# Optimization experiments

Measured on AMD Instinct MI355X. Metric: run time of the kernel, lower is better.

Reference implementation:

```python
import jax, jax.numpy as jnp
import numpy as np
from jax import lax

D_MODEL = 200
N_LAYER = 12
NHEADS = 8
HEADDIM = 50
D_STATE = 64
D_INNER = 2 * D_MODEL            # 400
CONV_DIM = D_INNER + 2 * D_STATE  # 528 (ngroups=1)
D_IN_PROJ = 2 * D_INNER + 2 * D_STATE + NHEADS  # 936
D_CONV = 4
EPS = 1e-5


def rmsnorm(x, w):
    v = jnp.mean(jnp.square(x), axis=-1, keepdims=True)
    return x * lax.rsqrt(v + EPS) * w


def groupnorm(x, groups, g, b):
    B, C, H, W = x.shape
    xg = x.reshape(B, groups, C // groups, H, W)
    mu = jnp.mean(xg, axis=(2, 3, 4), keepdims=True)
    var = jnp.mean(jnp.square(xg - mu), axis=(2, 3, 4), keepdims=True)
    xn = ((xg - mu) * lax.rsqrt(var + EPS)).reshape(B, C, H, W)
    return xn * g[:, None, None] + b[:, None, None]


def patch_embed(x, pe_conv_w, proj_in_w, gn_g, gn_b, spec_w):
    b, c, l, d = x.shape
    # time path: 'b c l d' -> (b, 1, c*l, d), conv -> (b, 25, c*l, 8)
    time_x = x.reshape(b, 1, c * l, d)
    t = lax.conv_general_dilated(time_x, proj_in_w, (1, 25), ((0, 0), (24, 24)),
                                 dimension_numbers=('NCHW', 'OIHW', 'NCHW'))
    t = jax.nn.gelu(groupnorm(t, 5, gn_g, gn_b), approximate=False)
    time_emb = t.transpose(0, 2, 1, 3).reshape(b, c, l, D_MODEL)
    # freq path: rfft over patch dim, norm='forward'
    spec = jnp.abs(jnp.fft.rfft(x, axis=-1, norm='forward'))  # (b,c,l,101)
    spec_emb = jnp.einsum('bclf,df->bcld', spec, spec_w)
    patch = time_emb + spec_emb
    # depthwise 7x7 positional conv over (d, c, l)
    pos = lax.conv_general_dilated(patch.transpose(0, 3, 1, 2), pe_conv_w, (1, 1),
                                   ((3, 3), (3, 3)),
                                   dimension_numbers=('NCHW', 'OIHW', 'NCHW'),
                                   feature_group_count=D_MODEL)
    return patch + pos.transpose(0, 2, 3, 1)


def ssd_scan(xh, dt, B, C, A, D):
    # xh: (b,l,h,p)  dt: (b,l,h)  B,C: (b,l,n)  A,D: (h,)
    b, l, h, p = xh.shape

    def step(state, inp):
        x_t, dt_t, B_t, C_t = inp
        dA = jnp.exp(dt_t * A)  # (b,h)
        state = state * dA[:, :, None, None] + \
            (dt_t[:, :, None, None] * x_t[:, :, :, None]) * B_t[:, None, None, :]
        y = jnp.einsum('bhpn,bn->bhp', state, C_t)
        return state, y

    state0 = jnp.zeros((b, h, p, D_STATE), xh.dtype)
    _, ys = lax.scan(step, state0,
                     (xh.transpose(1, 0, 2, 3), dt.transpose(1, 0, 2),
                      B.transpose(1, 0, 2), C.transpose(1, 0, 2)))
    return ys.transpose(1, 0, 2, 3) + xh * D[None, None, :, None]


def mamba2(u, in_w, conv_w, conv_b, dt_bias, A_log, D, gn_w, out_w):
    b, l, _ = u.shape
    zxbcdt = u @ in_w.T  # (b,l,936)
    z = zxbcdt[..., :D_INNER]
    xBC = zxbcdt[..., D_INNER:D_INNER + CONV_DIM]
    dt = jax.nn.softplus(zxbcdt[..., D_INNER + CONV_DIM:] + dt_bias)  # (b,l,8)
    # causal depthwise conv1d, kernel 4
    xc = lax.conv_general_dilated(xBC.transpose(0, 2, 1), conv_w, (1,), ((D_CONV - 1, 0),),
                                  dimension_numbers=('NCH', 'OIH', 'NCH'),
                                  feature_group_count=CONV_DIM)
    xBC = jax.nn.silu((xc + conv_b[:, None]).transpose(0, 2, 1))
    x = xBC[..., :D_INNER].reshape(b, l, NHEADS, HEADDIM)
    Bm = xBC[..., D_INNER:D_INNER + D_STATE]
    Cm = xBC[..., D_INNER + D_STATE:]
    y = ssd_scan(x, dt, Bm, Cm, -jnp.exp(A_log), D).reshape(b, l, D_INNER)
    y = rmsnorm(y * jax.nn.silu(z), gn_w)  # RMSNormGated, norm_before_gate=False
    return y @ out_w.T


@jax.checkpoint
def layer(hidden, residual, norm_w, in_w, conv_w, conv_b, dt_bias, A_log, D, gn_w, out_w):
    residual = hidden + residual
    hidden = mamba2(rmsnorm(residual, norm_w), in_w, conv_w, conv_b, dt_bias, A_log, D, gn_w, out_w)
    return hidden, residual


def forward(x, pe_conv_w, proj_in_w, gn_g, gn_b, spec_w, norm_w, in_proj_w, conv_w, conv_b,
            dt_bias, A_log, D, gnorm_w, out_proj_w, norm_f_w, head_w, head_b):
    b, c, l, d = x.shape
    hidden = patch_embed(x, pe_conv_w, proj_in_w, gn_g, gn_b, spec_w).reshape(b, c * l, d)
    residual = jnp.zeros_like(hidden)
    for i in range(N_LAYER):
        hidden, residual = layer(hidden, residual, norm_w[i], in_proj_w[i], conv_w[i],
                                 conv_b[i], dt_bias[i], A_log[i], D[i], gnorm_w[i], out_proj_w[i])
    hidden = rmsnorm(hidden + residual, norm_f_w).reshape(b, c, l, d)
    return hidden @ head_w.T + head_b


def setup_inputs():
    key = jax.random.key(0)
    ks = jax.random.split(key, 12)
    B, CH, L, P = 16, 19, 30, 200

    def g(k, shape, scale):
        return jax.random.normal(k, shape, jnp.float32) * scale

    dt = jax.random.uniform(ks[8], (N_LAYER, NHEADS), jnp.float32, 1e-3, 0.1)
    return {
        'x': g(ks[0], (B, CH, L, P), 1.0),
        'pe_conv_w': g(ks[1], (D_MODEL, 1, 7, 7), 0.15),
        'proj_in_w': g(ks[2], (25, 1, 1, 49), 0.14),
        'gn_g': jnp.ones(25, jnp.float32),
        'gn_b': jnp.zeros(25, jnp.float32),
        'spec_w': g(ks[3], (D_MODEL, 101), 0.1),
        'norm_w': jnp.ones((N_LAYER, D_MODEL), jnp.float32),
        'in_proj_w': g(ks[4], (N_LAYER, D_IN_PROJ, D_MODEL), 0.07),
        'conv_w': g(ks[5], (N_LAYER, CONV_DIM, 1, D_CONV), 0.4),
        'conv_b': jnp.zeros((N_LAYER, CONV_DIM), jnp.float32),
        'dt_bias': jnp.log(jnp.expm1(dt)),
        'A_log': jnp.log(jax.random.uniform(ks[9], (N_LAYER, NHEADS), jnp.float32, 1.0, 16.0)),
        'D': jnp.ones((N_LAYER, NHEADS), jnp.float32),
        'gnorm_w': jnp.ones((N_LAYER, D_INNER), jnp.float32),
        'out_proj_w': g(ks[6], (N_LAYER, D_MODEL, D_INNER), 0.05),
        'norm_f_w': jnp.ones(D_MODEL, jnp.float32),
        'head_w': g(ks[7], (D_MODEL, D_MODEL), 0.07),
        'head_b': jnp.zeros(D_MODEL, jnp.float32),
    }


def reference(x, pe_conv_w, proj_in_w, gn_g, gn_b, spec_w, norm_w, in_proj_w, conv_w, conv_b,
              dt_bias, A_log, D, gnorm_w, out_proj_w, norm_f_w, head_w, head_b):
    return forward(x, pe_conv_w, proj_in_w, gn_g, gn_b, spec_w, norm_w, in_proj_w, conv_w,
                   conv_b, dt_bias, A_log, D, gnorm_w, out_proj_w, norm_f_w, head_w, head_b)
```

## Files before the change

kernel.cpp:

```cpp
#include <hip/hip_runtime.h>
#include <hip/hip_bf16.h>
#include <math.h>

#define D_MODEL   200
#define N_LAYER   12
#define NHEADS    8
#define HEADDIM   50
#define D_STATE   64
#define D_INNER   400
#define CONV_DIM  528
#define D_IN_PROJ 936
#define D_CONV    4
#define EPS       1e-5f

#define BATCH 16
#define CH    19
#define LLEN  30
#define SEQ   570
#define NTOK  9120
#define NFREQ 101

typedef __attribute__((ext_vector_type(8))) short s8v;
typedef __attribute__((ext_vector_type(4))) float f32x4;

// ... 168 lines not shown
}

__global__ __launch_bounds__(256) void time_conv_kernel(
    const float* __restrict__ x, const float* __restrict__ pw,
    float* __restrict__ traw)
{
    int br = blockIdx.x;
    __shared__ float xr[200];
    if (threadIdx.x < 200) xr[threadIdx.x] = x[(size_t)br * 200 + threadIdx.x];
    __syncthreads();
    if (threadIdx.x < 200) {
        int oc = threadIdx.x >> 3, j = threadIdx.x & 7;
        int start = j * 25 - 24;
        float acc = 0.f;
#pragma unroll
        for (int k = 0; k < 49; k++) {
            int d = start + k;
            if (d >= 0 && d < 200) acc = fmaf(xr[d], pw[oc * 49 + k], acc);
        }
        int b = br / SEQ, row = br % SEQ;
        traw[(((size_t)b * 25 + oc) * SEQ + row) * 8 + j] = acc;
    }
}

__global__ __launch_bounds__(256) void gn_stats_kernel(
    const float* __restrict__ traw, float* __restrict__ stats)
{
    int bg = blockIdx.x;
    int b = bg / 5, g = bg % 5;
    const float* base = traw + ((size_t)b * 25 + g * 5) * SEQ * 8;
    float s = 0.f, q = 0.f;
    for (int i = threadIdx.x; i < 5 * SEQ * 8; i += 256) {
        float v = base[i];
        s += v; q = fmaf(v, v, q);
    }
    __shared__ float rs[4], rq[4];
    int lane = threadIdx.x & 63, w = threadIdx.x >> 6;
#pragma unroll
    for (int o = 32; o; o >>= 1) { s += __shfl_xor(s, o, 64); q += __shfl_xor(q, o, 64); }
    if (lane == 0) { rs[w] = s; rq[w] = q; }
    __syncthreads();
    if (threadIdx.x == 0) {
        float S = rs[0] + rs[1] + rs[2] + rs[3];
        float Q = rq[0] + rq[1] + rq[2] + rq[3];
        float inv = 1.f / (5.f * SEQ * 8.f);
        float mean = S * inv;
        float var = Q * inv - mean * mean;
        stats[bg * 2] = mean;
        stats[bg * 2 + 1] = rsqrtf(var + EPS);
    }
}

__global__ __launch_bounds__(256) void gn_gelu_kernel(
    const float* __restrict__ traw, const float* __restrict__ stats,
    const float* __restrict__ gn_g, const float* __restrict__ gn_b,
    float* __restrict__ patch)
{
    int idx = blockIdx.x * 256 + threadIdx.x;
    if (idx >= NTOK * 200) return;
    int d = idx % 200;
    int row = (idx / 200) % SEQ;
    int b = idx / (200 * SEQ);
    int oc = d >> 3, j = d & 7;
    float v = traw[(((size_t)b * 25 + oc) * SEQ + row) * 8 + j];
    int g = oc / 5;
    float mean = stats[(b * 5 + g) * 2];
    float rstd = stats[(b * 5 + g) * 2 + 1];
    v = (v - mean) * rstd * gn_g[oc] + gn_b[oc];
    float ge = 0.5f * v * (1.f + erff(v * 0.70710678118654752f));
    patch[idx] = ge;
}

__global__ __launch_bounds__(256) void dft_init_kernel(float* __restrict__ CS)
{
    int idx = blockIdx.x * 256 + threadIdx.x;
    if (idx >= 202 * 200) return;
    int f = idx / 200, d = idx % 200;
    int fr = (f < NFREQ) ? f : (f - NFREQ);
    int m = (fr * d) % 200;
    float ang = -6.283185307179586f * (float)m * (1.f / 200.f);
    CS[idx] = (f < NFREQ) ? cosf(ang) : sinf(ang);
}

__global__ __launch_bounds__(256) void dft_init_bf_kernel(short* __restrict__ CS)
{
    int idx = blockIdx.x * 256 + threadIdx.x;
    if (idx >= 202 * 224) return;
    int f = idx / 224, d = idx - f * 224;
    short out = 0;
    if (d < 200) {
        int fr = (f < NFREQ) ? f : (f - NFREQ);
        int m = (fr * d) % 200;
        float ang = -6.283185307179586f * (float)m * (1.f / 200.f);
        out = f2bf((f < NFREQ) ? cosf(ang) : sinf(ang));
    }
    CS[idx] = out;
}

__global__ __launch_bounds__(256) void mag_kernel(
    const float* __restrict__ cs_out, float* __restrict__ magv)
{
    int idx = blockIdx.x * 256 + threadIdx.x;
    if (idx >= NTOK * NFREQ) return;
    int m = idx / NFREQ, f = idx % NFREQ;
    float re = cs_out[(size_t)m * 202 + f];
    float im = cs_out[(size_t)m * 202 + NFREQ + f];
    magv[idx] = sqrtf(re * re + im * im) * 0.005f;
}

__global__ __launch_bounds__(256) void mag_bf_kernel(
    const float* __restrict__ cs_out, short* __restrict__ magv)
{
    int idx = blockIdx.x * 256 + threadIdx.x;
    if (idx >= NTOK * 128) return;
    int m = idx >> 7, f = idx & 127;
    short out = 0;
    if (f < NFREQ) {
        float re = cs_out[(size_t)m * 202 + f];
        float im = cs_out[(size_t)m * 202 + NFREQ + f];
        out = f2bf(sqrtf(re * re + im * im) * 0.005f);
    }
    magv[idx] = out;
}

__global__ __launch_bounds__(256) void pe_conv3_kernel(
    const float* __restrict__ patch, const float* __restrict__ pw,
    float* __restrict__ hidden)
{
    int b = blockIdx.x, dc = blockIdx.y, ct = blockIdx.z;
    int d0 = dc * 16, c0 = ct * 4;
    __shared__ float pl[10 * 30 * 16];
    __shared__ float wl[49 * 16];
    int tid = threadIdx.x;
    int dd = tid & 15;
    int d = d0 + dd;

    for (int i = tid; i < 10 * 30 * 16; i += 256) {
        int ddl = i & 15, r = i >> 4;
        int l = r % 30, cr = r / 30;
        int cc = c0 + cr - 3, dl = d0 + ddl;
        pl[i] = (cc >= 0 && cc < CH && dl < 200)
                    ? patch[((size_t)(b * CH + cc) * LLEN + l) * 200 + dl] : 0.f;
    }
    for (int i = tid; i < 49 * 16; i += 256) {
        int k = i >> 4, dl = d0 + (i & 15);
        wl[i] = (dl < 200) ? pw[(size_t)dl * 49 + k] : 0.f;
    }
    __syncthreads();

    float wreg[49];
#pragma unroll
    for (int k = 0; k < 49; k++) wreg[k] = wl[k * 16 + dd];

    for (int o = tid; o < 4 * 30 * 16; o += 256) {
        int r2 = o >> 4;
        int l = r2 % 30, ci = r2 / 30;
        int c = c0 + ci;
        if (c >= CH) continue;
        float acc = pl[((ci + 3) * 30 + l) * 16 + dd];
#pragma unroll
        for (int i = 0; i < 7; i++) {
#pragma unroll
            for (int j = 0; j < 7; j++) {
                int ll = l + j - 3;
                if (ll < 0 || ll >= LLEN) continue;
                acc = fmaf(pl[((ci + i) * 30 + ll) * 16 + dd], wreg[i * 7 + j], acc);
            }
        }
        if (d < 200) hidden[((size_t)(b * CH + c) * LLEN + l) * 200 + d] = acc;
    }
}

__global__ __launch_bounds__(64) void add_rmsnorm_kernel(
    const float* __restrict__ hidden, float* __restrict__ residual,
    const float* __restrict__ wn, float* __restrict__ u,
    short* __restrict__ ubf, int first)
{
    int m = blockIdx.x;
    int lane = threadIdx.x;
    const float* hr = hidden + (size_t)m * 200;
    float* rr = residual + (size_t)m * 200;
    float v[4];
    float ss = 0.f;
#pragma unroll
    for (int i = 0; i < 4; i++) {
        int k = lane + i * 64;
        float xv = 0.f;
        if (k < 200) {
            xv = hr[k] + (first ? 0.f : rr[k]);
            rr[k] = xv;
        }
        v[i] = xv;
        ss = fmaf(xv, xv, ss);
    }
#pragma unroll
    for (int o = 32; o; o >>= 1) ss += __shfl_xor(ss, o, 64);
    float rstd = rsqrtf(ss * (1.f / 200.f) + EPS);
#pragma unroll
    for (int i = 0; i < 4; i++) {
        int k = lane + i * 64;
        float val = v[i] * rstd * ((k < 200) ? wn[k] : 0.f);
        if (k < 200 && u) u[(size_t)m * 200 + k] = val;
        if (ubf) {
            if (k < 200) ubf[(size_t)m * 224 + k] = f2bf(val);
            else if (k < 224) ubf[(size_t)m * 224 + k] = 0;
        }
    }
}

__global__ __launch_bounds__(256) void norm_dt_kernel(
    const float* __restrict__ hidden, float* __restrict__ residual,
    const float* __restrict__ wn, short* __restrict__ ubf,
    const float* __restrict__ Win, const float* __restrict__ dt_bias,
    float* __restrict__ dtb, int layer, int first)
{
    int m = blockIdx.x;
    int tid = threadIdx.x;
    __shared__ float su[200];
    __shared__ float rs[4];
    float xv = 0.f;
    if (tid < 200) {
        xv = hidden[(size_t)m * 200 + tid] + (first ? 0.f : residual[(size_t)m * 200 + tid]);
        residual[(size_t)m * 200 + tid] = xv;
    }
    float ss = xv * xv;
#pragma unroll
    for (int o = 32; o; o >>= 1) ss += __shfl_xor(ss, o, 64);
    int lane = tid & 63, w = tid >> 6;
    if (lane == 0) rs[w] = ss;
    __syncthreads();
    float rstd = rsqrtf((rs[0] + rs[1] + rs[2] + rs[3]) * (1.f / 200.f) + EPS);
    if (tid < 200) {
        float val = xv * rstd * wn[tid];
        su[tid] = val;
        ubf[(size_t)m * 224 + tid] = f2bf(val);
    } else if (tid < 224) {
        ubf[(size_t)m * 224 + tid] = 0;
    }
    __syncthreads();
    int h = tid >> 5, l = tid & 31;
    const float* wr = Win + (size_t)layer * D_IN_PROJ * 200 + (size_t)(928 + h) * 200;
    float s = 0.f;
    for (int k = l; k < 200; k += 32) s = fmaf(su[k], wr[k], s);
    s += __shfl_xor(s, 16, 32);
    s += __shfl_xor(s, 8, 32);
    s += __shfl_xor(s, 4, 32);
    s += __shfl_xor(s, 2, 32);
    s += __shfl_xor(s, 1, 32);
    if (l == 0) {
        float raw = s + dt_bias[layer * NHEADS + h];
        dtb[(size_t)m * NHEADS + h] = (raw > 20.f) ? raw : log1pf(expf(raw));
    }
}

__global__ __launch_bounds__(256) void dt_gemv_kernel(
    const float* __restrict__ u, const float* __restrict__ Win,
    const float* __restrict__ dt_bias, float* __restrict__ dtb, int layer)
{
    int tid = threadIdx.x;
    int tok = blockIdx.x * 4 + (tid >> 6);
    int head = (tid >> 3) & 7;
    int l8 = tid & 7;
    const float* ur = u + (size_t)tok * 200;
    const float* wr = Win + (size_t)layer * D_IN_PROJ * 200 + (size_t)(928 + head) * 200;
    float s = 0.f;
    for (int k = l8; k < 200; k += 8) s = fmaf(ur[k], wr[k], s);
    s += __shfl_xor(s, 1, 64);
    s += __shfl_xor(s, 2, 64);
    s += __shfl_xor(s, 4, 64);
    if (l8 == 0) {
        float raw = s + dt_bias[layer * NHEADS + head];
        dtb[(size_t)tok * NHEADS + head] = (raw > 20.f) ? raw : log1pf(expf(raw));
    }
}

__global__ __launch_bounds__(256) void dtconv2_kernel(
    const float* __restrict__ zxbcdt, const float* __restrict__ cw,
    const float* __restrict__ cb, float* __restrict__ xBC, int layer)
{
    int b = blockIdx.x, tt = blockIdx.y;
    int t0 = tt * 8;
    __shared__ float zs[11][528];
    const float* cwl = cw + (size_t)layer * CONV_DIM * 4;
    const float* cbl = cb + (size_t)layer * CONV_DIM;
    for (int i = threadIdx.x; i < 11 * 528; i += 256) {
        int r = i / 528, ch = i - r * 528;
        int t = t0 - 3 + r;
        zs[r][ch] = (t >= 0 && t < SEQ)
                        ? zxbcdt[(size_t)(b * SEQ + t) * D_IN_PROJ + D_INNER + ch] : 0.f;
    }
    __syncthreads();
    for (int o = threadIdx.x; o < 8 * 528; o += 256) {
        int tr = o / 528, ch = o - tr * 528;
        int t = t0 + tr;
        if (t >= SEQ) continue;
        float acc = cbl[ch];
#pragma unroll
        for (int k = 0; k < 4; k++)
            acc = fmaf(zs[tr + k][ch], cwl[ch * 4 + k], acc);
        xBC[(size_t)(b * SEQ + t) * CONV_DIM + ch] = acc / (1.f + __expf(-acc));
    }
}

__global__ __launch_bounds__(256) void ssd_state4_kernel(
    const float* __restrict__ xBC, const float* __restrict__ dtb,
    const float* __restrict__ A_log, float* __restrict__ Sbuf,
    float* __restrict__ Pd, int layer, int lchunk, int nchunk)
{
    int b = blockIdx.x, c = blockIdx.y, bz = blockIdx.z;
    int tid = threadIdx.x;
    int hl = tid >> 6, p = tid & 63;
    int h = bz * 4 + hl;
    float A = -expf(A_log[layer * NHEADS + h]);

    __shared__ __align__(16) float sh[2][2][272];
    int t0 = c * lchunk;
    int npairs = lchunk >> 1, rem = lchunk & 1;

    {
        if (tid < 132) {
            int tok = (tid >= 66) ? 1 : 0;
            int fidx = tid - tok * 66;
            int g = (fidx < 50) ? (50 * bz + fidx) : (fidx + 50);
            float4 v = ((const float4*)(xBC + (size_t)(b * SEQ + t0 + tok) * CONV_DIM))[g];
            *(float4*)&sh[0][tok][fidx * 4] = v;
        } else if (tid < 140) {
            int e = tid - 132, tok = e >> 2, hd = e & 3;
            sh[0][tok][264 + hd] = dtb[(size_t)(b * SEQ + t0 + tok) * NHEADS + bz * 4 + hd];
        }
    }
    __syncthreads();

    float s[64];
#pragma unroll
    for (int n = 0; n < 64; n++) s[n] = 0.f;
    float pacc = 1.f;

    for (int i = 0; i < npairs; i++) {
        int t = t0 + 2 * i;
        int buf = i & 1, nb = buf ^ 1;
        bool pf = (2 * i + 2 < lchunk);
        float4 rx;
        float rdt = 0.f;
        int tok = 0, fidx = 0;
        if (pf) {
            if (tid < 132) {
                tok = (tid >= 66) ? 1 : 0;
                fidx = tid - tok * 66;
                int tq = t + 2 + tok; if (tq > SEQ - 1) tq = SEQ - 1;
                int g = (fidx < 50) ? (50 * bz + fidx) : (fidx + 50);
                rx = ((const float4*)(xBC + (size_t)(b * SEQ + tq) * CONV_DIM))[g];
            } else if (tid < 140) {
                int e = tid - 132, tk = e >> 2, hd = e & 3;
                int tq = t + 2 + tk; if (tq > SEQ - 1) tq = SEQ - 1;
                rdt = dtb[(size_t)(b * SEQ + tq) * NHEADS + bz * 4 + hd];
            }
        }
#pragma unroll
        for (int k = 0; k < 2; k++) {
            float dtv = sh[buf][k][264 + hl];
            float xp  = (p < HEADDIM) ? sh[buf][k][hl * HEADDIM + p] : 0.f;
            float dA = __expf(dtv * A);
            float u  = dtv * xp;
            pacc *= dA;
            const float4* B4 = (const float4*)&sh[buf][k][200];
#pragma unroll
            for (int n4 = 0; n4 < 16; n4++) {
                float4 bq = B4[n4];
                s[4 * n4 + 0] = fmaf(s[4 * n4 + 0], dA, u * bq.x);
                s[4 * n4 + 1] = fmaf(s[4 * n4 + 1], dA, u * bq.y);
                s[4 * n4 + 2] = fmaf(s[4 * n4 + 2], dA, u * bq.z);
                s[4 * n4 + 3] = fmaf(s[4 * n4 + 3], dA, u * bq.w);
            }
        }
        if (pf) {
            if (tid < 132) *(float4*)&sh[nb][tok][fidx * 4] = rx;
            else if (tid < 140) { int e = tid - 132; sh[nb][e >> 2][264 + (e & 3)] = rdt; }
        }
        __syncthreads();
    }

    if (rem) {
        int buf = npairs & 1;
        float dtv = sh[buf][0][264 + hl];
        float xp  = (p < HEADDIM) ? sh[buf][0][hl * HEADDIM + p] : 0.f;
        float dA = __expf(dtv * A);
        float u  = dtv * xp;
        pacc *= dA;
        const float4* B4 = (const float4*)&sh[buf][0][200];
#pragma unroll
        for (int n4 = 0; n4 < 16; n4++) {
            float4 bq = B4[n4];
            s[4 * n4 + 0] = fmaf(s[4 * n4 + 0], dA, u * bq.x);
            s[4 * n4 + 1] = fmaf(s[4 * n4 + 1], dA, u * bq.y);
            s[4 * n4 + 2] = fmaf(s[4 * n4 + 2], dA, u * bq.z);
            s[4 * n4 + 3] = fmaf(s[4 * n4 + 3], dA, u * bq.w);
        }
    }

    if (p < HEADDIM) {
        float* Sb = Sbuf + ((size_t)((b * NHEADS + h) * nchunk + c)) * (HEADDIM * 64)
                    + p * 64;
#pragma unroll
        for (int n4 = 0; n4 < 16; n4++)
            ((float4*)Sb)[n4] = make_float4(s[4 * n4], s[4 * n4 + 1],
                                            s[4 * n4 + 2], s[4 * n4 + 3]);
    }
    if (p == 0) Pd[(b * NHEADS + h) * nchunk + c] = pacc;
}

__global__ __launch_bounds__(512) void ssd_state_kernel(
    const float* __restrict__ xBC, const float* __restrict__ dtb,
    const float* __restrict__ A_log, float* __restrict__ Sbuf,
    float* __restrict__ Pd, int layer, int lchunk, int nchunk)
{
    int b = blockIdx.x, c = blockIdx.y;
    int tid = threadIdx.x;
    int h = tid >> 6, p = tid & 63;
    float A = -expf(A_log[layer * NHEADS + h]);

    __shared__ float sh[2][544];
    int t0 = c * lchunk, tend = t0 + lchunk;

    {
        const float* base = xBC + (size_t)(b * SEQ + t0) * CONV_DIM;
        sh[0][tid] = base[tid];
        if (tid < 24) {
            int e2 = 512 + tid;
            sh[0][e2] = (e2 < 528) ? base[e2]
                                   : dtb[(size_t)(b * SEQ + t0) * NHEADS + (e2 - 528)];
        }
    }
    __syncthreads();

    float s[64];
#pragma unroll
    for (int n = 0; n < 64; n++) s[n] = 0.f;
    float pacc = 1.f;

    for (int t = t0; t < tend; t++) {
        int cur = (t - t0) & 1, nxt = cur ^ 1;
        float pf0 = 0.f, pf1 = 0.f;
        if (t + 1 < tend) {
            const float* base = xBC + (size_t)(b * SEQ + t + 1) * CONV_DIM;
            pf0 = base[tid];
            if (tid < 24) {
                int e2 = 512 + tid;
                pf1 = (e2 < 528) ? base[e2]
                                 : dtb[(size_t)(b * SEQ + t + 1) * NHEADS + (e2 - 528)];
            }
        }
        float dtv = sh[cur][528 + h];
        float xp  = (p < HEADDIM) ? sh[cur][h * HEADDIM + p] : 0.f;
        float dA = __expf(dtv * A);
        float u  = dtv * xp;
        pacc *= dA;
        const float4* B4 = (const float4*)&sh[cur][D_INNER];
#pragma unroll
        for (int n4 = 0; n4 < 16; n4++) {
            float4 bq = B4[n4];
            s[4 * n4 + 0] = fmaf(s[4 * n4 + 0], dA, u * bq.x);
            s[4 * n4 + 1] = fmaf(s[4 * n4 + 1], dA, u * bq.y);
            s[4 * n4 + 2] = fmaf(s[4 * n4 + 2], dA, u * bq.z);
            s[4 * n4 + 3] = fmaf(s[4 * n4 + 3], dA, u * bq.w);
        }
        if (t + 1 < tend) {
            sh[nxt][tid] = pf0;
            if (tid < 24) sh[nxt][512 + tid] = pf1;
        }
        __syncthreads();
    }

    if (p < HEADDIM) {
        float* Sb = Sbuf + ((size_t)((b * NHEADS + h) * nchunk + c)) * (HEADDIM * 64)
                    + p * 64;
#pragma unroll
        for (int n4 = 0; n4 < 16; n4++)
            ((float4*)Sb)[n4] = make_float4(s[4 * n4], s[4 * n4 + 1],
                                            s[4 * n4 + 2], s[4 * n4 + 3]);
    }
    if (p == 0) Pd[(b * NHEADS + h) * nchunk + c] = pacc;
}

__global__ __launch_bounds__(256) void ssd_scan2b_kernel(
    float* __restrict__ Sbuf, const float* __restrict__ Pd, int nchunk)
{
    int bh = blockIdx.x;
    int e = blockIdx.y * 256 + threadIdx.x;
    if (e >= HEADDIM * 64) return;
    float* base = Sbuf + (size_t)bh * nchunk * (HEADDIM * 64) + e;
    const float* pd = Pd + bh * nchunk;
    float cur = 0.f;
    for (int c = 0; c < nchunk; c++) {
        float l = base[(size_t)c * (HEADDIM * 64)];
        base[(size_t)c * (HEADDIM * 64)] = cur;
        cur = fmaf(pd[c], cur, l);
    }
}

__global__ __launch_bounds__(256) void ssd_out5_kernel(
    const float* __restrict__ xBC, const float* __restrict__ dtb,
    const float* __restrict__ zxbcdt, const float* __restrict__ A_log,
    const float* __restrict__ Dv, const float* __restrict__ Sbuf,
    const float* __restrict__ gw, short* __restrict__ ybf,
    float* __restrict__ ssq, int layer, int lchunk, int nchunk)
{
    int b = blockIdx.x, c = blockIdx.y, bz = blockIdx.z;
    int tid = threadIdx.x;
    int hl = tid >> 6, p = tid & 63;
    int h = bz * 4 + hl;
    float A = -expf(A_log[layer * NHEADS + h]);
    float Dh = Dv[layer * NHEADS + h];
    float gval = (p < HEADDIM) ? gw[(size_t)layer * D_INNER + h * HEADDIM + p] : 0.f;

    __shared__ __align__(16) float sh[2][2][336];
    __shared__ __align__(16) float shz[2][2][200];
    __shared__ float red[2][2][4];
    int t0 = c * lchunk;
    int npairs = lchunk >> 1;

    {
        if (tid < 164) {
            int tok = (tid >= 82) ? 1 : 0;
            int fidx = tid - tok * 82;
            int g = (fidx < 50) ? (50 * bz + fidx) : (fidx + 50);
            float4 v = ((const float4*)(xBC + (size_t)(b * SEQ + t0 + tok) * CONV_DIM))[g];
            *(float4*)&sh[0][tok][fidx * 4] = v;
        } else if (tid < 172) {
            int e = tid - 164, tok = e >> 2, hd = e & 3;
            sh[0][tok][328 + hd] = dtb[(size_t)(b * SEQ + t0 + tok) * NHEADS + bz * 4 + hd];
        }
        if (tid < 100) {
            int tok = (tid >= 50) ? 1 : 0;
            int fz = tid - tok * 50;
            float4 v = ((const float4*)(zxbcdt + (size_t)(b * SEQ + t0 + tok) * D_IN_PROJ))[50 * bz + fz];
            *(float4*)&shz[0][tok][fz * 4] = v;
        }
    }

    float s[64];
    if (p < HEADDIM) {
        const float* Sb = Sbuf + ((size_t)((b * NHEADS + h) * nchunk + c)) * (HEADDIM * 64)
                          + p * 64;
#pragma unroll
        for (int n4 = 0; n4 < 16; n4++) {
            float4 v = ((const float4*)Sb)[n4];
            s[4 * n4] = v.x; s[4 * n4 + 1] = v.y; s[4 * n4 + 2] = v.z; s[4 * n4 + 3] = v.w;
        }
    } else {
#pragma unroll
        for (int n = 0; n < 64; n++) s[n] = 0.f;
    }
    __syncthreads();

    for (int i = 0; i < npairs; i++) {
        int t = t0 + 2 * i;
        int buf = i & 1, nb = buf ^ 1;
        bool pf = (2 * i + 2 < lchunk);
        float4 rx, rz;
        float rdt = 0.f;
        int xtok = 0, xf = 0, ztok = 0, zf = 0;
        if (pf) {
            if (tid < 164) {
                xtok = (tid >= 82) ? 1 : 0;
                xf = tid - xtok * 82;
                int tq = t + 2 + xtok; if (tq > SEQ - 1) tq = SEQ - 1;
                int g = (xf < 50) ? (50 * bz + xf) : (xf + 50);
                rx = ((const float4*)(xBC + (size_t)(b * SEQ + tq) * CONV_DIM))[g];
            } else if (tid < 172) {
                int e = tid - 164, tk = e >> 2, hd = e & 3;
                int tq = t + 2 + tk; if (tq > SEQ - 1) tq = SEQ - 1;
                rdt = dtb[(size_t)(b * SEQ + tq) * NHEADS + bz * 4 + hd];
            }
            if (tid < 100) {
                ztok = (tid >= 50) ? 1 : 0;
                zf = tid - ztok * 50;
                int tq = t + 2 + ztok; if (tq > SEQ - 1) tq = SEQ - 1;
                rz = ((const float4*)(zxbcdt + (size_t)(b * SEQ + tq) * D_IN_PROJ))[50 * bz + zf];
            }
        }
        float g0 = 0.f, g1 = 0.f;
#pragma unroll
        for (int k = 0; k < 2; k++) {
            float dtv = sh[buf][k][328 + hl];
            float xp  = (p < HEADDIM) ? sh[buf][k][hl * HEADDIM + p] : 0.f;
            float dA = __expf(dtv * A);
            float u  = dtv * xp;
            const float4* B4 = (const float4*)&sh[buf][k][200];
            const float4* C4 = (const float4*)&sh[buf][k][264];
            float y0 = 0.f, y1 = 0.f, y2 = 0.f, y3 = 0.f;
#pragma unroll
            for (int n4 = 0; n4 < 16; n4++) {
                float4 bq = B4[n4];
                float4 cq = C4[n4];
                float t0v = fmaf(s[4 * n4 + 0], dA, u * bq.x);
                float t1v = fmaf(s[4 * n4 + 1], dA, u * bq.y);
                float t2v = fmaf(s[4 * n4 + 2], dA, u * bq.z);
                float t3v = fmaf(s[4 * n4 + 3], dA, u * bq.w);
                s[4 * n4 + 0] = t0v; s[4 * n4 + 1] = t1v;
                s[4 * n4 + 2] = t2v; s[4 * n4 + 3] = t3v;
                y0 = fmaf(t0v, cq.x, y0);
                y1 = fmaf(t1v, cq.y, y1);
                y2 = fmaf(t2v, cq.z, y2);
                y3 = fmaf(t3v, cq.w, y3);
            }
            if (p < HEADDIM) {
                float yv = fmaf(xp, Dh, (y0 + y1) + (y2 + y3));
                float zv = shz[buf][k][hl * HEADDIM + p];
                float g = yv * (zv / (1.f + __expf(-zv)));
                if (k == 0) g0 = g; else g1 = g;
            }
        }
        size_t row0 = (size_t)(b * SEQ + t) * 416;
        size_t row1 = row0 + 416;
        if (p < HEADDIM) {
            ybf[row0 + h * HEADDIM + p] = f2bf(g0 * gval);
            ybf[row1 + h * HEADDIM + p] = f2bf(g1 * gval);
        } else {
            int widx = h * 14 + (p - HEADDIM);
            if (widx < 16) {
                ybf[row0 + 400 + widx] = 0;
                ybf[row1 + 400 + widx] = 0;
            }
        }
        float gs0 = g0 * g0, gs1 = g1 * g1;
#pragma unroll
        for (int o = 32; o; o >>= 1) {
            gs0 += __shfl_xor(gs0, o, 64);
            gs1 += __shfl_xor(gs1, o, 64);
        }
        if (p == 0) { red[buf][0][hl] = gs0; red[buf][1][hl] = gs1; }
        if (pf) {
            if (tid < 164) *(float4*)&sh[nb][xtok][xf * 4] = rx;
            else if (tid < 172) { int e = tid - 164; sh[nb][e >> 2][328 + (e & 3)] = rdt; }
            if (tid < 100) *(float4*)&shz[nb][ztok][zf * 4] = rz;
        }
        __syncthreads();
        if (tid == 0) {
            ssq[(size_t)(b * SEQ + t) * 2 + bz] =
                (red[buf][0][0] + red[buf][0][1]) + (red[buf][0][2] + red[buf][0][3]);
            ssq[(size_t)(b * SEQ + t + 1) * 2 + bz] =
                (red[buf][1][0] + red[buf][1][1]) + (red[buf][1][2] + red[buf][1][3]);
        }
    }
}

__global__ __launch_bounds__(256) void rstd_kernel(
    const float* __restrict__ ssq, float* __restrict__ rstdb)
{
    int m = blockIdx.x * 256 + threadIdx.x;
    if (m >= NTOK) return;
    rstdb[m] = rsqrtf((ssq[2 * m] + ssq[2 * m + 1]) * (1.f / D_INNER) + EPS);
}

__global__ __launch_bounds__(512) void ssd_out_kernel(
    const float* __restrict__ xBC, const float* __restrict__ dtb,
    const float* __restrict__ A_log, const float* __restrict__ Dv,
    const float* __restrict__ Sbuf, float* __restrict__ y,
    int layer, int lchunk, int nchunk)
{
    int b = blockIdx.x, c = blockIdx.y;
    int tid = threadIdx.x;
    int h = tid >> 6, p = tid & 63;
    float A = -expf(A_log[layer * NHEADS + h]);
    float Dh = Dv[layer * NHEADS + h];

    __shared__ float sh[2][544];
    int t0 = c * lchunk, tend = t0 + lchunk;

    {
        const float* base = xBC + (size_t)(b * SEQ + t0) * CONV_DIM;
        sh[0][tid] = base[tid];
        if (tid < 24) {
            int e2 = 512 + tid;
            sh[0][e2] = (e2 < 528) ? base[e2]
                                   : dtb[(size_t)(b * SEQ + t0) * NHEADS + (e2 - 528)];
        }
    }

    float s[64];
    if (p < HEADDIM) {
        const float* Sb = Sbuf + ((size_t)((b * NHEADS + h) * nchunk + c)) * (HEADDIM * 64)
                          + p * 64;
#pragma unroll
        for (int n4 = 0; n4 < 16; n4++) {
            float4 v = ((const float4*)Sb)[n4];
            s[4 * n4] = v.x; s[4 * n4 + 1] = v.y; s[4 * n4 + 2] = v.z; s[4 * n4 + 3] = v.w;
        }
    } else {
#pragma unroll
        for (int n = 0; n < 64; n++) s[n] = 0.f;
    }
    __syncthreads();

    for (int t = t0; t < tend; t++) {
        int cur = (t - t0) & 1, nxt = cur ^ 1;
        float pf0 = 0.f, pf1 = 0.f;
        if (t + 1 < tend) {
            const float* base = xBC + (size_t)(b * SEQ + t + 1) * CONV_DIM;
            pf0 = base[tid];
            if (tid < 24) {
                int e2 = 512 + tid;
                pf1 = (e2 < 528) ? base[e2]
                                 : dtb[(size_t)(b * SEQ + t + 1) * NHEADS + (e2 - 528)];
            }
        }
        float dtv = sh[cur][528 + h];
        float xp  = (p < HEADDIM) ? sh[cur][h * HEADDIM + p] : 0.f;
        float dA = __expf(dtv * A);
        float u  = dtv * xp;
        const float4* B4 = (const float4*)&sh[cur][D_INNER];
        const float4* C4 = (const float4*)&sh[cur][D_INNER + D_STATE];
        float y0 = 0.f, y1 = 0.f, y2 = 0.f, y3 = 0.f;
#pragma unroll
        for (int n4 = 0; n4 < 16; n4++) {
            float4 bq = B4[n4];
            float4 cq = C4[n4];
            float t0v = fmaf(s[4 * n4 + 0], dA, u * bq.x);
            float t1v = fmaf(s[4 * n4 + 1], dA, u * bq.y);
            float t2v = fmaf(s[4 * n4 + 2], dA, u * bq.z);
            float t3v = fmaf(s[4 * n4 + 3], dA, u * bq.w);
            s[4 * n4 + 0] = t0v; s[4 * n4 + 1] = t1v;
            s[4 * n4 + 2] = t2v; s[4 * n4 + 3] = t3v;
            y0 = fmaf(t0v, cq.x, y0);
            y1 = fmaf(t1v, cq.y, y1);
            y2 = fmaf(t2v, cq.z, y2);
            y3 = fmaf(t3v, cq.w, y3);
        }
        if (p < HEADDIM) {
            float yv = (y0 + y1) + (y2 + y3);
            y[(size_t)(b * SEQ + t) * D_INNER + h * HEADDIM + p] = fmaf(xp, Dh, yv);
        }
        if (t + 1 < tend) {
            sh[nxt][tid] = pf0;
            if (tid < 24) sh[nxt][512 + tid] = pf1;
        }
        __syncthreads();
    }
}

__global__ __launch_bounds__(256) void gate_norm_kernel(
    float* __restrict__ y, const float* __restrict__ zxbcdt,
    const float* __restrict__ gw, short* __restrict__ ybf, int layer)
{
    int m = blockIdx.x;
    __shared__ float buf[D_INNER];
    __shared__ float red[4];
    const float* z = zxbcdt + (size_t)m * D_IN_PROJ;
    float* yr = y + (size_t)m * D_INNER;
    const float* gwl = gw + (size_t)layer * D_INNER;
    float ss = 0.f;
    for (int k = threadIdx.x; k < D_INNER; k += 256) {
        float zv = z[k];
        float sz = zv / (1.f + expf(-zv));
        float g = yr[k] * sz;
        buf[k] = g;
        ss = fmaf(g, g, ss);
    }
    int lane = threadIdx.x & 63, w = threadIdx.x >> 6;
#pragma unroll
    for (int o = 32; o; o >>= 1) ss += __shfl_xor(ss, o, 64);
    if (lane == 0) red[w] = ss;
    __syncthreads();
    float tot = red[0] + red[1] + red[2] + red[3];
    float rstd = rsqrtf(tot * (1.f / D_INNER) + EPS);
    for (int k = threadIdx.x; k < 416; k += 256) {
        if (k < D_INNER) {
            float v = buf[k] * rstd * gwl[k];
            yr[k] = v;
            if (ybf) ybf[(size_t)m * 416 + k] = f2bf(v);
        } else if (ybf) {
            ybf[(size_t)m * 416 + k] = 0;
        }
    }
}

extern "C" void kernel_launch(void* const* d_in, const int* in_sizes, int n_in,
                              void* d_out, int out_size, void* d_ws, size_t ws_size,
                              hipStream_t stream)
{
    const float* x         = (const float*)d_in[0];
    const float* pe_conv_w = (const float*)d_in[1];
    const float* proj_in_w = (const float*)d_in[2];
    const float* gn_g      = (const float*)d_in[3];
    const float* gn_b      = (const float*)d_in[4];
    const float* spec_w    = (const float*)d_in[5];
    const float* norm_w    = (const float*)d_in[6];
    const float* in_proj_w = (const float*)d_in[7];
    const float* conv_w    = (const float*)d_in[8];
    const float* conv_b    = (const float*)d_in[9];
    const float* dt_bias   = (const float*)d_in[10];
    const float* A_log     = (const float*)d_in[11];
    const float* Dv        = (const float*)d_in[12];
    const float* gnorm_w   = (const float*)d_in[13];
    const float* out_proj_w= (const float*)d_in[14];
    const float* norm_f_w  = (const float*)d_in[15];
    const float* head_w    = (const float*)d_in[16];
    const float* head_b    = (const float*)d_in[17];
    float* out = (float*)d_out;
    float* ws  = (float*)d_ws;

    const size_t needA = 27956704ull * sizeof(float);
    int fast = (ws_size >= needA) ? 1 : 0;

    int nchunk, lchunk;
    float *residual = ws, *hidden = ws + 1824000;
    float *zxbcdt, *xBC, *dtb, *Sbuf, *Pd;
    float *ubuf = nullptr, *ybuf = nullptr, *ssq = nullptr, *rstdb = nullptr;
    short *w_in_bf = nullptr, *w_out_bf = nullptr, *w_head_bf = nullptr,
          *w_spec_bf = nullptr, *csmat_bf = nullptr, *x_bf = nullptr,
          *ubuf_bf = nullptr, *ybuf_bf = nullptr, *magb_bf = nullptr;

    if (fast) {
        nchunk = 15; lchunk = 38;
        zxbcdt = ws + 3648000;
        xBC    = ws + 12184320;
        dtb    = ws + 16999680;
        Sbuf   = ws + 17072640;
        Pd     = ws + 23216640;
        short* pool = (short*)(ws + 23218560);
        w_in_bf   = pool;
        w_out_bf  = pool + 2515968;
        w_head_bf = pool + 3514368;
        w_spec_bf = pool + 3559168;
        ubuf_bf   = pool + 3584768;
        ybuf_bf   = pool + 5627648;
        ssq       = ws + 27929344;
        rstdb     = ws + 27947584;
        csmat_bf  = (short*)(Sbuf + 4000000);
        x_bf      = (short*)(Sbuf + 4100000);
        magb_bf   = (short*)(Sbuf + 5200000);
    } else {
        nchunk = 6; lchunk = 95;
        ubuf   = ws + 3648000;
        zxbcdt = ws + 5472000;
        xBC    = ws + 14008320;
        dtb    = ws + 18823680;
        ybuf   = ws + 18896640;
        Sbuf   = ws + 1824000;
        Pd     = ws + 5470000;
    }

    float* traw  = fast ? Sbuf : ybuf;
    float* patch = zxbcdt;
    float* csout = fast ? (Sbuf + 2000000) : (xBC + 50000);
    float* csmat = xBC;
    float* magb  = fast ? nullptr : (xBC + 2000000);
    float* stats = dtb;

    if (fast) {
        cast_pad_kernel<<<(12 * 936 * 224 + 255) / 256, 256, 0, stream>>>(
            in_proj_w, w_in_bf, 12 * 936, 200, 224);
        cast_pad_kernel<<<(12 * 200 * 416 + 255) / 256, 256, 0, stream>>>(
            out_proj_w, w_out_bf, 12 * 200, 400, 416);
        cast_pad_kernel<<<(200 * 224 + 255) / 256, 256, 0, stream>>>(
            head_w, w_head_bf, 200, 200, 224);
        cast_pad_kernel<<<(200 * 128 + 255) / 256, 256, 0, stream>>>(
            spec_w, w_spec_bf, 200, 101, 128);
        cast_pad_kernel<<<(9120 * 224 + 255) / 256, 256, 0, stream>>>(
            x, x_bf, 9120, 200, 224);
        dft_init_bf_kernel<<<(202 * 224 + 255) / 256, 256, 0, stream>>>(csmat_bf);
    } else {
        dft_init_kernel<<<(202 * 200 + 255) / 256, 256, 0, stream>>>(csmat);
    }

    time_conv_kernel<<<NTOK, 256, 0, stream>>>(x, proj_in_w, traw);
    gn_stats_kernel<<<80, 256, 0, stream>>>(traw, stats);
    gn_gelu_kernel<<<(NTOK * 200 + 255) / 256, 256, 0, stream>>>(traw, stats, gn_g, gn_b, patch);
    if (fast) {
        gemm_bf16<<<dim3(2, 72), 256, 0, stream>>>(x_bf, csmat_bf, nullptr, nullptr, csout,
                                                   NTOK, 202, 224, 0);
        mag_bf_kernel<<<(NTOK * 128 + 255) / 256, 256, 0, stream>>>(csout, magb_bf);
        gemm_bf16<<<dim3(2, 72), 256, 0, stream>>>(magb_bf, w_spec_bf, nullptr, nullptr, patch,
                                                   NTOK, 200, 128, 1);
    } else {
        gemm_nt<<<dim3(2, 72), 256, 0, stream>>>(x, csmat, nullptr, csout, NTOK, 202, 200, 0);
        mag_kernel<<<(NTOK * NFREQ + 255) / 256, 256, 0, stream>>>(csout, magb);
        gemm_nt<<<dim3(2, 72), 256, 0, stream>>>(magb, spec_w, nullptr, patch,
                                                 NTOK, 200, NFREQ, 1);
    }
    pe_conv3_kernel<<<dim3(16, 13, 5), 256, 0, stream>>>(patch, pe_conv_w, hidden);

    for (int i = 0; i < N_LAYER; i++) {
        if (fast) {
            norm_dt_kernel<<<NTOK, 256, 0, stream>>>(hidden, residual, norm_w + i * 200,
                                                     ubuf_bf, in_proj_w, dt_bias, dtb,
                                                     i, (i == 0) ? 1 : 0);
            gemm_bf16<<<dim3(8, 72), 256, 0, stream>>>(
                ubuf_bf, w_in_bf + (size_t)i * 936 * 224, nullptr, nullptr, zxbcdt,
                NTOK, D_IN_PROJ, 224, 0);
        } else {
            add_rmsnorm_kernel<<<NTOK, 64, 0, stream>>>(hidden, residual, norm_w + i * 200,
                                                        ubuf, nullptr, (i == 0) ? 1 : 0);
            dt_gemv_kernel<<<NTOK / 4, 256, 0, stream>>>(ubuf, in_proj_w, dt_bias, dtb, i);
            gemm_nt<<<dim3(8, 72), 256, 0, stream>>>(
                ubuf, in_proj_w + (size_t)i * D_IN_PROJ * 200, nullptr, zxbcdt,
                NTOK, D_IN_PROJ, 200, 0);
        }
        dtconv2_kernel<<<dim3(16, 72), 256, 0, stream>>>(zxbcdt, conv_w, conv_b, xBC, i);
        {
            dim3 g(BATCH, nchunk);
            if (fast) {
                ssd_state4_kernel<<<dim3(BATCH, nchunk, 2), 256, 0, stream>>>(
                    xBC, dtb, A_log, Sbuf, Pd, i, lchunk, nchunk);
                ssd_scan2b_kernel<<<dim3(BATCH * NHEADS, 13), 256, 0, stream>>>(Sbuf, Pd, nchunk);
                ssd_out5_kernel<<<dim3(BATCH, nchunk, 2), 256, 0, stream>>>(
                    xBC, dtb, zxbcdt, A_log, Dv, Sbuf, gnorm_w, ybuf_bf, ssq,
                    i, lchunk, nchunk);
                rstd_kernel<<<(NTOK + 255) / 256, 256, 0, stream>>>(ssq, rstdb);
                gemm_bf16<<<dim3(2, 72), 256, 0, stream>>>(
                    ybuf_bf, w_out_bf + (size_t)i * 200 * 416, nullptr, rstdb, hidden,
                    NTOK, 200, 416, 0);
            } else {
                ssd_state_kernel<<<g, 512, 0, stream>>>(xBC, dtb, A_log, Sbuf, Pd,
                                                        i, lchunk, nchunk);
                ssd_scan2b_kernel<<<dim3(BATCH * NHEADS, 13), 256, 0, stream>>>(Sbuf, Pd, nchunk);
                ssd_out_kernel<<<g, 512, 0, stream>>>(xBC, dtb, A_log, Dv, Sbuf, ybuf,
                                                      i, lchunk, nchunk);
                gate_norm_kernel<<<NTOK, 256, 0, stream>>>(ybuf, zxbcdt, gnorm_w, nullptr, i);
                gemm_nt<<<dim3(2, 72), 256, 0, stream>>>(
                    ybuf, out_proj_w + (size_t)i * 200 * D_INNER, nullptr, hidden,
                    NTOK, 200, D_INNER, 0);
            }
        }
    }

    add_rmsnorm_kernel<<<NTOK, 64, 0, stream>>>(hidden, residual, norm_f_w,
                                                fast ? nullptr : ubuf,
                                                fast ? ubuf_bf : nullptr, 0);
    if (fast) {
        gemm_bf16<<<dim3(2, 72), 256, 0, stream>>>(ubuf_bf, w_head_bf, head_b, nullptr, out,
                                                   NTOK, 200, 224, 0);
    } else {
        gemm_nt<<<dim3(2, 72), 256, 0, stream>>>(ubuf, head_w, head_b, out,
                                                 NTOK, 200, 200, 0);
    }
}
```

Before: 2.433 ms.

## Drop LDS double-buffering in SSD scan kernels; read tokens directly from global

The chunked SSD state and output kernels no longer stage two tokens at a time through double-buffered shared memory with a block barrier per pair. Each 64-thread head group now streams x, B, C, dt and z straight from global memory, one token per iteration, with no __syncthreads. The per-token sum of squares is written per head (8 values per token) rather than combined across heads in shared memory, and rstd_kernel now sums those 8 partials. This removes barriers and LDS traffic but relies on cache hits for the broadcast B/C loads and loses explicit prefetch, so more global load latency is exposed per step.

Result: slower. 2.888 ms (+18.7%).

```diff
diff --git a/kernel.cpp b/kernel.cpp
--- a/kernel.cpp
+++ b/kernel.cpp
@@ -494,7 +494,7 @@
     }
 }
 
-__global__ __launch_bounds__(256) void ssd_state4_kernel(
+__global__ __launch_bounds__(256) void ssd_state6_kernel(
     const float* __restrict__ xBC, const float* __restrict__ dtb,
     const float* __restrict__ A_log, float* __restrict__ Sbuf,
     float* __restrict__ Pd, int layer, int lchunk, int nchunk)
@@ -505,81 +505,23 @@
     int h = bz * 4 + hl;
     float A = -expf(A_log[layer * NHEADS + h]);
 
-    __shared__ __align__(16) float sh[2][2][272];
-    int t0 = c * lchunk;
-    int npairs = lchunk >> 1, rem = lchunk & 1;
-
-    {
-        if (tid < 132) {
-            int tok = (tid >= 66) ? 1 : 0;
-            int fidx = tid - tok * 66;
-            int g = (fidx < 50) ? (50 * bz + fidx) : (fidx + 50);
-            float4 v = ((const float4*)(xBC + (size_t)(b * SEQ + t0 + tok) * CONV_DIM))[g];
-            *(float4*)&sh[0][tok][fidx * 4] = v;
-        } else if (tid < 140) {
-            int e = tid - 132, tok = e >> 2, hd = e & 3;
-            sh[0][tok][264 + hd] = dtb[(size_t)(b * SEQ + t0 + tok) * NHEADS + bz * 4 + hd];
-        }
-    }
-    __syncthreads();
-
+    int t0 = c * lchunk, tend = t0 + lchunk;
     float s[64];
 #pragma unroll
     for (int n = 0; n < 64; n++) s[n] = 0.f;
     float pacc = 1.f;
 
-    for (int i = 0; i < npairs; i++) {
-        int t = t0 + 2 * i;
-        int buf = i & 1, nb = buf ^ 1;
-        bool pf = (2 * i + 2 < lchunk);
-        float4 rx;
-        float rdt = 0.f;
-        int tok = 0, fidx = 0;
-        if (pf) {
-            if (tid < 132) {
-                tok = (tid >= 66) ? 1 : 0;
-                fidx = tid - tok * 66;
-                int tq = t + 2 + tok; if (tq > SEQ - 1) tq = SEQ - 1;
-                int g = (fidx < 50) ? (50 * bz + fidx) : (fidx + 50);
-                rx = ((const float4*)(xBC + (size_t)(b * SEQ + tq) * CONV_DIM))[g];
-            } else if (tid < 140) {
-                int e = tid - 132, tk = e >> 2, hd = e & 3;
-                int tq = t + 2 + tk; if (tq > SEQ - 1) tq = SEQ - 1;
-                rdt = dtb[(size_t)(b * SEQ + tq) * NHEADS + bz * 4 + hd];
-            }
-        }
-#pragma unroll
-        for (int k = 0; k < 2; k++) {
-            float dtv = sh[buf][k][264 + hl];
-            float xp  = (p < HEADDIM) ? sh[buf][k][hl * HEADDIM + p] : 0.f;
-            float dA = __expf(dtv * A);
-            float u  = dtv * xp;
-            pacc *= dA;
-            const float4* B4 = (const float4*)&sh[buf][k][200];
-#pragma unroll
-            for (int n4 = 0; n4 < 16; n4++) {
-                float4 bq = B4[n4];
-                s[4 * n4 + 0] = fmaf(s[4 * n4 + 0], dA, u * bq.x);
-                s[4 * n4 + 1] = fmaf(s[4 * n4 + 1], dA, u * bq.y);
-                s[4 * n4 + 2] = fmaf(s[4 * n4 + 2], dA, u * bq.z);
-                s[4 * n4 + 3] = fmaf(s[4 * n4 + 3], dA, u * bq.w);
-            }
-        }
-        if (pf) {
-            if (tid < 132) *(float4*)&sh[nb][tok][fidx * 4] = rx;
-            else if (tid < 140) { int e = tid - 132; sh[nb][e >> 2][264 + (e & 3)] = rdt; }
-        }
-        __syncthreads();
-    }
-
-    if (rem) {
-        int buf = npairs & 1;
-        float dtv = sh[buf][0][264 + hl];
-        float xp  = (p < HEADDIM) ? sh[buf][0][hl * HEADDIM + p] : 0.f;
+    const float* xrow  = xBC + (size_t)(b * SEQ + t0) * CONV_DIM;
+    const float* dtrow = dtb + (size_t)(b * SEQ + t0) * NHEADS + h;
+
+    for (int t = t0; t < tend; t++) {
+        float dtv = *dtrow;
+        float xp  = xrow[h * HEADDIM + p];
+        xp = (p < HEADDIM) ? xp : 0.f;
         float dA = __expf(dtv * A);
         float u  = dtv * xp;
         pacc *= dA;
-        const float4* B4 = (const float4*)&sh[buf][0][200];
+        const float4* B4 = (const float4*)(xrow + D_INNER);
 #pragma unroll
         for (int n4 = 0; n4 < 16; n4++) {
             float4 bq = B4[n4];
@@ -588,6 +530,8 @@
             s[4 * n4 + 2] = fmaf(s[4 * n4 + 2], dA, u * bq.z);
             s[4 * n4 + 3] = fmaf(s[4 * n4 + 3], dA, u * bq.w);
         }
+        xrow += CONV_DIM;
+        dtrow += NHEADS;
     }
 
     if (p < HEADDIM) {
@@ -690,7 +634,7 @@
     }
 }
 
-__global__ __launch_bounds__(256) void ssd_out5_kernel(
+__global__ __launch_bounds__(256) void ssd_out6_kernel(
     const float* __restrict__ xBC, const float* __restrict__ dtb,
     const float* __restrict__ zxbcdt, const float* __restrict__ A_log,
     const float* __restrict__ Dv, const float* __restrict__ Sbuf,
@@ -705,30 +649,7 @@
     float Dh = Dv[layer * NHEADS + h];
     float gval = (p < HEADDIM) ? gw[(size_t)layer * D_INNER + h * HEADDIM + p] : 0.f;
 
-    __shared__ __align__(16) float sh[2][2][336];
-    __shared__ __align__(16) float shz[2][2][200];
-    __shared__ float red[2][2][4];
-    int t0 = c * lchunk;
-    int npairs = lchunk >> 1;
-
-    {
-        if (tid < 164) {
-            int tok = (tid >= 82) ? 1 : 0;
-            int fidx = tid - tok * 82;
-            int g = (fidx < 50) ? (50 * bz + fidx) : (fidx + 50);
-            float4 v = ((const float4*)(xBC + (size_t)(b * SEQ + t0 + tok) * CONV_DIM))[g];
-            *(float4*)&sh[0][tok][fidx * 4] = v;
-        } else if (tid < 172) {
-            int e = tid - 164, tok = e >> 2, hd = e & 3;
-            sh[0][tok][328 + hd] = dtb[(size_t)(b * SEQ + t0 + tok) * NHEADS + bz * 4 + hd];
-        }
-        if (tid < 100) {
-            int tok = (tid >= 50) ? 1 : 0;
-            int fz = tid - tok * 50;
-            float4 v = ((const float4*)(zxbcdt + (size_t)(b * SEQ + t0 + tok) * D_IN_PROJ))[50 * bz + fz];
-            *(float4*)&shz[0][tok][fz * 4] = v;
-        }
-    }
+    int t0 = c * lchunk, tend = t0 + lchunk;
 
     float s[64];
     if (p < HEADDIM) {
@@ -743,97 +664,56 @@
 #pragma unroll
         for (int n = 0; n < 64; n++) s[n] = 0.f;
     }
-    __syncthreads();
-
-    for (int i = 0; i < npairs; i++) {
-        int t = t0 + 2 * i;
-        int buf = i & 1, nb = buf ^ 1;
-        bool pf = (2 * i + 2 < lchunk);
-        float4 rx, rz;
-        float rdt = 0.f;
-        int xtok = 0, xf = 0, ztok = 0, zf = 0;
-        if (pf) {
-            if (tid < 164) {
-                xtok = (tid >= 82) ? 1 : 0;
-                xf = tid - xtok * 82;
-                int tq = t + 2 + xtok; if (tq > SEQ - 1) tq = SEQ - 1;
-                int g = (xf < 50) ? (50 * bz + xf) : (xf + 50);
-                rx = ((const float4*)(xBC + (size_t)(b * SEQ + tq) * CONV_DIM))[g];
-            } else if (tid < 172) {
-                int e = tid - 164, tk = e >> 2, hd = e & 3;
-                int tq = t + 2 + tk; if (tq > SEQ - 1) tq = SEQ - 1;
-                rdt = dtb[(size_t)(b * SEQ + tq) * NHEADS + bz * 4 + hd];
-            }
-            if (tid < 100) {
-                ztok = (tid >= 50) ? 1 : 0;
-                zf = tid - ztok * 50;
-                int tq = t + 2 + ztok; if (tq > SEQ - 1) tq = SEQ - 1;
-                rz = ((const float4*)(zxbcdt + (size_t)(b * SEQ + tq) * D_IN_PROJ))[50 * bz + zf];
-            }
-        }
-        float g0 = 0.f, g1 = 0.f;
-#pragma unroll
-        for (int k = 0; k < 2; k++) {
-            float dtv = sh[buf][k][328 + hl];
-            float xp  = (p < HEADDIM) ? sh[buf][k][hl * HEADDIM + p] : 0.f;
-            float dA = __expf(dtv * A);
-            float u  = dtv * xp;
-            const float4* B4 = (const float4*)&sh[buf][k][200];
-            const float4* C4 = (const float4*)&sh[buf][k][264];
-            float y0 = 0.f, y1 = 0.f, y2 = 0.f, y3 = 0.f;
-#pragma unroll
-            for (int n4 = 0; n4 < 16; n4++) {
-                float4 bq = B4[n4];
-                float4 cq = C4[n4];
-                float t0v = fmaf(s[4 * n4 + 0], dA, u * bq.x);
-                float t1v = fmaf(s[4 * n4 + 1], dA, u * bq.y);
-                float t2v = fmaf(s[4 * n4 + 2], dA, u * bq.z);
-                float t3v = fmaf(s[4 * n4 + 3], dA, u * bq.w);
-                s[4 * n4 + 0] = t0v; s[4 * n4 + 1] = t1v;
-                s[4 * n4 + 2] = t2v; s[4 * n4 + 3] = t3v;
-                y0 = fmaf(t0v, cq.x, y0);
-                y1 = fmaf(t1v, cq.y, y1);
-                y2 = fmaf(t2v, cq.z, y2);
-                y3 = fmaf(t3v, cq.w, y3);
-            }
-            if (p < HEADDIM) {
-                float yv = fmaf(xp, Dh, (y0 + y1) + (y2 + y3));
-                float zv = shz[buf][k][hl * HEADDIM + p];
-                float g = yv * (zv / (1.f + __expf(-zv)));
-                if (k == 0) g0 = g; else g1 = g;
-            }
+
+    const float* xrow  = xBC + (size_t)(b * SEQ + t0) * CONV_DIM;
+    const float* zrow  = zxbcdt + (size_t)(b * SEQ + t0) * D_IN_PROJ;
+    const float* dtrow = dtb + (size_t)(b * SEQ + t0) * NHEADS + h;
+
+    for (int t = t0; t < tend; t++) {
+        float dtv = *dtrow;
+        float xp  = xrow[h * HEADDIM + p];
+        xp = (p < HEADDIM) ? xp : 0.f;
+        float zv  = zrow[h * HEADDIM + p];
+        float dA = __expf(dtv * A);
+        float u  = dtv * xp;
+        const float4* B4 = (const float4*)(xrow + D_INNER);
+        const float4* C4 = (const float4*)(xrow + D_INNER + D_STATE);
+        float y0 = 0.f, y1 = 0.f, y2 = 0.f, y3 = 0.f;
+#pragma unroll
+        for (int n4 = 0; n4 < 16; n4++) {
+            float4 bq = B4[n4];
+            float4 cq = C4[n4];
+            float t0v = fmaf(s[4 * n4 + 0], dA, u * bq.x);
+            float t1v = fmaf(s[4 * n4 + 1], dA, u * bq.y);
+            float t2v = fmaf(s[4 * n4 + 2], dA, u * bq.z);
+            float t3v = fmaf(s[4 * n4 + 3], dA, u * bq.w);
+            s[4 * n4 + 0] = t0v; s[4 * n4 + 1] = t1v;
+            s[4 * n4 + 2] = t2v; s[4 * n4 + 3] = t3v;
+            y0 = fmaf(t0v, cq.x, y0);
+            y1 = fmaf(t1v, cq.y, y1);
+            y2 = fmaf(t2v, cq.z, y2);
+            y3 = fmaf(t3v, cq.w, y3);
+        }
+        float g0 = 0.f;
+        if (p < HEADDIM) {
+            float yv = fmaf(xp, Dh, (y0 + y1) + (y2 + y3));
+            g0 = yv * (zv / (1.f + __expf(-zv)));
         }
         size_t row0 = (size_t)(b * SEQ + t) * 416;
-        size_t row1 = row0 + 416;
         if (p < HEADDIM) {
             ybf[row0 + h * HEADDIM + p] = f2bf(g0 * gval);
-            ybf[row1 + h * HEADDIM + p] = f2bf(g1 * gval);
         } else {
             int widx = h * 14 + (p - HEADDIM);
-            if (widx < 16) {
-                ybf[row0 + 400 + widx] = 0;
-                ybf[row1 + 400 + widx] = 0;
-            }
-        }
-        float gs0 = g0 * g0, gs1 = g1 * g1;
-#pragma unroll
-        for (int o = 32; o; o >>= 1) {
-            gs0 += __shfl_xor(gs0, o, 64);
-            gs1 += __shfl_xor(gs1, o, 64);
-        }
-        if (p == 0) { red[buf][0][hl] = gs0; red[buf][1][hl] = gs1; }
-        if (pf) {
-            if (tid < 164) *(float4*)&sh[nb][xtok][xf * 4] = rx;
-            else if (tid < 172) { int e = tid - 164; sh[nb][e >> 2][328 + (e & 3)] = rdt; }
-            if (tid < 100) *(float4*)&shz[nb][ztok][zf * 4] = rz;
-        }
-        __syncthreads();
-        if (tid == 0) {
-            ssq[(size_t)(b * SEQ + t) * 2 + bz] =
-                (red[buf][0][0] + red[buf][0][1]) + (red[buf][0][2] + red[buf][0][3]);
-            ssq[(size_t)(b * SEQ + t + 1) * 2 + bz] =
-                (red[buf][1][0] + red[buf][1][1]) + (red[buf][1][2] + red[buf][1][3]);
-        }
+            if (widx < 16) ybf[row0 + 400 + widx] = 0;
+        }
+        float gs0 = g0 * g0;
+#pragma unroll
+        for (int o = 32; o; o >>= 1) gs0 += __shfl_xor(gs0, o, 64);
+        if (p == 0) ssq[(size_t)(b * SEQ + t) * NHEADS + h] = gs0;
+
+        xrow += CONV_DIM;
+        zrow += D_IN_PROJ;
+        dtrow += NHEADS;
     }
 }
 
@@ -842,7 +722,10 @@
 {
     int m = blockIdx.x * 256 + threadIdx.x;
     if (m >= NTOK) return;
-    rstdb[m] = rsqrtf((ssq[2 * m] + ssq[2 * m + 1]) * (1.f / D_INNER) + EPS);
+    const float4* q = (const float4*)(ssq + (size_t)m * NHEADS);
+    float4 a = q[0], bq = q[1];
+    float tot = ((a.x + a.y) + (a.z + a.w)) + ((bq.x + bq.y) + (bq.z + bq.w));
+    rstdb[m] = rsqrtf(tot * (1.f / D_INNER) + EPS);
 }
 
 __global__ __launch_bounds__(512) void ssd_out_kernel(
@@ -992,7 +875,7 @@
     float* out = (float*)d_out;
     float* ws  = (float*)d_ws;
 
-    const size_t needA = 27956704ull * sizeof(float);
+    const size_t needA = 28011424ull * sizeof(float);
     int fast = (ws_size >= needA) ? 1 : 0;
 
     int nchunk, lchunk;
@@ -1018,7 +901,7 @@
         ubuf_bf   = pool + 3584768;
         ybuf_bf   = pool + 5627648;
         ssq       = ws + 27929344;
-        rstdb     = ws + 27947584;
+        rstdb     = ws + 28002304;
         csmat_bf  = (short*)(Sbuf + 4000000);
         x_bf      = (short*)(Sbuf + 4100000);
         magb_bf   = (short*)(Sbuf + 5200000);
@@ -1093,10 +976,10 @@
         {
             dim3 g(BATCH, nchunk);
             if (fast) {
-                ssd_state4_kernel<<<dim3(BATCH, nchunk, 2), 256, 0, stream>>>(
+                ssd_state6_kernel<<<dim3(BATCH, nchunk, 2), 256, 0, stream>>>(
                     xBC, dtb, A_log, Sbuf, Pd, i, lchunk, nchunk);
                 ssd_scan2b_kernel<<<dim3(BATCH * NHEADS, 13), 256, 0, stream>>>(Sbuf, Pd, nchunk);
-                ssd_out5_kernel<<<dim3(BATCH, nchunk, 2), 256, 0, stream>>>(
+                ssd_out6_kernel<<<dim3(BATCH, nchunk, 2), 256, 0, stream>>>(
                     xBC, dtb, zxbcdt, A_log, Dv, Sbuf, gnorm_w, ybuf_bf, ssq,
                     i, lchunk, nchunk);
                 rstd_kernel<<<(NTOK + 255) / 256, 256, 0, stream>>>(ssq, rstdb);
```
